# Kernel optimization log

Hardware: AMD Instinct MI355X
Metric: run time of the kernel (lower is better)

The kernel has to match this reference:

```python
import jax, jax.numpy as jnp
import numpy as np
import math

B, T, D, H, L = 64, 255, 512, 8, 8
CODEBOOK = 512
V = CODEBOOK + 3  # bos/eos/pad
COND_DIM = 512
MAX_LEN = 256
HD = D // H


def _layernorm(x, g, b, eps=1e-5):
    mu = jnp.mean(x, axis=-1, keepdims=True)
    var = jnp.mean(jnp.square(x - mu), axis=-1, keepdims=True)
    return (x - mu) * jax.lax.rsqrt(var + eps) * g + b


def setup_inputs() -> dict:
    key = jax.random.key(0)
    ks = jax.random.split(key, 24)
    s = 0.02
    d = {
        'tokens': jax.random.randint(ks[0], (B, T), 0, V),
        'cond': jax.random.normal(ks[1], (B, COND_DIM), jnp.float32),
        'emb': jax.random.normal(ks[2], (V, D), jnp.float32) * s,  # tied token_emb / head weight
        'pos_emb': jax.random.normal(ks[3], (1, MAX_LEN, D), jnp.float32) * s,
        'cond_w1': jax.random.normal(ks[4], (COND_DIM, D), jnp.float32) * s,
        'cond_b1': jnp.zeros((D,), jnp.float32),
        'cond_w2': jax.random.normal(ks[5], (D, D), jnp.float32) * s,
        'cond_b2': jnp.zeros((D,), jnp.float32),
        'ln1_g': jnp.ones((L, D), jnp.float32),
        'ln1_b': jnp.zeros((L, D), jnp.float32),
        'qkv_w': jax.random.normal(ks[6], (L, D, 3 * D), jnp.float32) * s,
        'qkv_b': jnp.zeros((L, 3 * D), jnp.float32),
        'proj_w': jax.random.normal(ks[7], (L, D, D), jnp.float32) * s,
        'proj_b': jnp.zeros((L, D), jnp.float32),
        'ln2_g': jnp.ones((L, D), jnp.float32),
        'ln2_b': jnp.zeros((L, D), jnp.float32),
        'mlp_w1': jax.random.normal(ks[8], (L, D, 4 * D), jnp.float32) * s,
        'mlp_b1': jnp.zeros((L, 4 * D), jnp.float32),
        'mlp_w2': jax.random.normal(ks[9], (L, 4 * D, D), jnp.float32) * s,
        'mlp_b2': jnp.zeros((L, D), jnp.float32),
        'lnf_g': jnp.ones((D,), jnp.float32),
        'lnf_b': jnp.zeros((D,), jnp.float32),
    }
    return d


def reference(tokens, cond, emb, pos_emb, cond_w1, cond_b1, cond_w2, cond_b2,
              ln1_g, ln1_b, qkv_w, qkv_b, proj_w, proj_b,
              ln2_g, ln2_b, mlp_w1, mlp_b1, mlp_w2, mlp_b2, lnf_g, lnf_b):
    b, t = tokens.shape
    h = emb[tokens] + pos_emb[:, :t, :]                              # [B,T,D]
    c = jax.nn.silu(cond @ cond_w1 + cond_b1) @ cond_w2 + cond_b2    # [B,D]
    h = jnp.concatenate([c[:, None, :], h], axis=1)                  # [B,S,D]
    S = t + 1
    causal = jnp.tril(jnp.ones((S, S), bool))
    scale = 1.0 / math.sqrt(HD)
    for i in range(L):
        x = _layernorm(h, ln1_g[i], ln1_b[i])
        qkv = (x @ qkv_w[i] + qkv_b[i]).reshape(b, S, 3, H, HD).transpose(2, 0, 3, 1, 4)
        q, k, v = qkv[0], qkv[1], qkv[2]                             # [B,H,S,hd]
        a = jnp.einsum('bhsd,bhtd->bhst', q, k) * scale
        a = jnp.where(causal, a, -jnp.inf)
        a = jax.nn.softmax(a, axis=-1)
        o = jnp.einsum('bhst,bhtd->bhsd', a, v).transpose(0, 2, 1, 3).reshape(b, S, D)
        h = h + o @ proj_w[i] + proj_b[i]
        x = _layernorm(h, ln2_g[i], ln2_b[i])
        h = h + jax.nn.gelu(x @ mlp_w1[i] + mlp_b1[i], approximate=False) @ mlp_w2[i] + mlp_b2[i]
    h = _layernorm(h, lnf_g, lnf_b)
    return (h @ emb.T)[:, 1:, :]                                     # [B,T,V]
```

## Files before the change

kernel.cpp:

```cpp
#include <hip/hip_runtime.h>
#include <hip/hip_bf16.h>

typedef __attribute__((ext_vector_type(8))) short bf16x8;
typedef __attribute__((ext_vector_type(4))) float f32x4;
typedef __attribute__((ext_vector_type(4))) unsigned short u16x4;
typedef __attribute__((ext_vector_type(8))) unsigned short u16x8;
typedef unsigned short u16;

#define DEV static __device__ __forceinline__

DEV float bf2f(u16 u) {
  union { unsigned int i; float f; } c; c.i = ((unsigned int)u) << 16; return c.f;
}
DEV u16 f2bf(float f) {
  union { float f; unsigned int i; } c; c.f = f;
  unsigned int i = c.i;
  i += 0x7FFFu + ((i >> 16) & 1u);
  return (u16)(i >> 16);
}

DEV void gload_lds16(const void* g, void* l) {
  __builtin_amdgcn_global_load_lds((const __attribute__((address_space(1))) void*)g,
                                   (__attribute__((address_space(3))) void*)l, 16, 0, 0);
}

DEV f32x4 mfma16(bf16x8 a, bf16x8 b, f32x4 c) {
  return __builtin_amdgcn_mfma_f32_16x16x32_bf16(a, b, c, 0, 0, 0);
}

DEV float fasterf(float x) {
  float ax = fabsf(x);
  float t = 1.0f / (1.0f + 0.3275911f * ax);
  float y = t * (0.254829592f + t * (-0.284496736f + t * (1.421413741f +
            t * (-1.453152027f + t * 1.061405429f))));
  float r = 1.0f - y * __expf(-ax * ax);
  return copysignf(r, x);
}
DEV float gelu(float v) { return 0.5f * v * (1.0f + fasterf(v * 0.70710678118f)); }

__global__ __launch_bounds__(256) void ktranspose(const float* __restrict__ in, u16* __restrict__ out,
                                                  int K, int N) {
  __shared__ u16 tile[32][33];
  const float* src = in + (size_t)blockIdx.z * K * N;
  u16* dst = out + (size_t)blockIdx.z * K * N;
  const int n0 = blockIdx.x * 32, k0 = blockIdx.y * 32;
  const int tx = threadIdx.x, ty = threadIdx.y;
#pragma unroll
  for (int i = ty; i < 32; i += 8) tile[i][tx] = f2bf(src[(size_t)(k0 + i) * N + n0 + tx]);
  __syncthreads();
#pragma unroll
  for (int i = ty; i < 32; i += 8) dst[(size_t)(n0 + i) * K + k0 + tx] = tile[tx][i];
}

__global__ __launch_bounds__(256) void kcvt(const float* __restrict__ in, u16* __restrict__ out, int n) {
  int i = blockIdx.x * 256 + threadIdx.x;
  if (i < n) out[i] = f2bf(in[i]);
}

__global__ __launch_bounds__(256) void kcond(const float* __restrict__ cond, const float* __restrict__ w1,
                                             const float* __restrict__ b1, const float* __restrict__ w2,
                                             const float* __restrict__ b2, float* __restrict__ h) {
  __shared__ float xr[512];
  __shared__ float t1[512];
  const int b = blockIdx.x, tid = threadIdx.x;
  for (int i = tid; i < 512; i += 256) xr[i] = cond[b * 512 + i];
  __syncthreads();
  for (int j = tid; j < 512; j += 256) {
    float acc = b1[j];
    for (int k = 0; k < 512; ++k) acc += xr[k] * w1[k * 512 + j];
    t1[j] = acc / (1.f + __expf(-acc));
  }
  __syncthreads();
  for (int j = tid; j < 512; j += 256) {
    float acc = b2[j];
    for (int k = 0; k < 512; ++k) acc += t1[k] * w2[k * 512 + j];
    h[(size_t)b * 256 * 512 + j] = acc;
  }
}

__global__ __launch_bounds__(256) void kembed(const int* __restrict__ tok, const float* __restrict__ emb,
                                              const float* __restrict__ pos, float* __restrict__ h) {
  const int idx = blockIdx.x;
  const int b = idx / 255, t = idx % 255;
  const int c = threadIdx.x * 2;
  const int tk = tok[idx];
  float2 ev = *(const float2*)(emb + (size_t)tk * 512 + c);
  float2 pv = *(const float2*)(pos + (size_t)t * 512 + c);
  float2 r;
  r.x = ev.x + pv.x;
  r.y = ev.y + pv.y;
  *(float2*)(h + ((size_t)b * 256 + 1 + t) * 512 + c) = r;
}

__global__ __launch_bounds__(256) void kln(const float* __restrict__ hin, const float* __restrict__ g,
                                           const float* __restrict__ bt, u16* __restrict__ out) {
  const int row = blockIdx.x * 4 + (threadIdx.x >> 6), lane = threadIdx.x & 63;
  const float4* x = (const float4*)(hin + (size_t)row * 512);
  float4 v0 = x[lane], v1 = x[lane + 64];
  float s1 = v0.x + v0.y + v0.z + v0.w + v1.x + v1.y + v1.z + v1.w;
  float s2 = v0.x * v0.x + v0.y * v0.y + v0.z * v0.z + v0.w * v0.w +
             v1.x * v1.x + v1.y * v1.y + v1.z * v1.z + v1.w * v1.w;
#pragma unroll
  for (int off = 1; off < 64; off <<= 1) { s1 += __shfl_xor(s1, off); s2 += __shfl_xor(s2, off); }
  float mu = s1 * (1.f / 512.f);
  float var = s2 * (1.f / 512.f) - mu * mu;
  float rs = rsqrtf(var + 1e-5f);
  const int c0 = lane * 4;
  float4 g0 = *(const float4*)(g + c0), g1 = *(const float4*)(g + 256 + c0);
  float4 b0 = *(const float4*)(bt + c0), b1 = *(const float4*)(bt + 256 + c0);
  u16x4 o0, o1;
  o0[0] = f2bf((v0.x - mu) * rs * g0.x + b0.x);
  o0[1] = f2bf((v0.y - mu) * rs * g0.y + b0.y);
  o0[2] = f2bf((v0.z - mu) * rs * g0.z + b0.z);
  o0[3] = f2bf((v0.w - mu) * rs * g0.w + b0.w);
  o1[0] = f2bf((v1.x - mu) * rs * g1.x + b1.x);
  o1[1] = f2bf((v1.y - mu) * rs * g1.y + b1.y);
  o1[2] = f2bf((v1.z - mu) * rs * g1.z + b1.z);
  o1[3] = f2bf((v1.w - mu) * rs * g1.w + b1.w);
  *(u16x4*)(out + (size_t)row * 512 + c0) = o0;
  *(u16x4*)(out + (size_t)row * 512 + 256 + c0) = o1;
}

template<int MODE>
__global__ __launch_bounds__(256, 2) void kgemm3(const u16* __restrict__ A, const u16* __restrict__ Bt,
                                                 const float* __restrict__ bias, void* __restrict__ Cout,
                                                 int M, int N, int K) {
  __shared__ __align__(16) u16 As[3][4096];
  __shared__ __align__(16) u16 Bs[3][4096];
  const int tid = threadIdx.x;
  const int lane = tid & 63;
  const int wr = tid >> 7, wc = (tid >> 6) & 1;
  const int m0 = blockIdx.x * 128, n0 = blockIdx.y * 128;
  const int nkt = K >> 5;
  const size_t Kb = (size_t)K * 2;

  const int srow = tid >> 2;
  const int schunk = tid & 3;
  const int sc = schunk ^ ((srow >> 1) & 3);
  const int d1 = tid * 16, d2 = tid * 16 + 4096;
  int brA = n0 + srow, brB = n0 + srow + 64;
  if (MODE == 3) { brA = min(brA, N - 1); brB = min(brB, N - 1); }
  const char* Ab = (const char*)A;
  const char* Bb = (const char*)Bt;
  const size_t a0 = (size_t)(m0 + srow) * Kb + sc * 16;
  const size_t a1 = (size_t)(m0 + srow + 64) * Kb + sc * 16;
  const size_t b0 = (size_t)brA * Kb + sc * 16;
  const size_t b1 = (size_t)brB * Kb + sc * 16;

  f32x4 acc[4][4];
#pragma unroll
  for (int i = 0; i < 4; ++i)
#pragma unroll
    for (int j = 0; j < 4; ++j) acc[i][j] = f32x4{0.f, 0.f, 0.f, 0.f};

#pragma unroll
  for (int t = 0; t < 2; ++t) {
    const size_t ko = (size_t)t * 64;
    gload_lds16(Ab + a0 + ko, (char*)As[t] + d1);
    gload_lds16(Ab + a1 + ko, (char*)As[t] + d2);
    gload_lds16(Bb + b0 + ko, (char*)Bs[t] + d1);
    gload_lds16(Bb + b1 + ko, (char*)Bs[t] + d2);
  }
  asm volatile("s_waitcnt vmcnt(4)" ::: "memory");
  __builtin_amdgcn_s_barrier();
  __builtin_amdgcn_sched_barrier(0);

  const int kchunk = (((lane >> 4) ^ ((lane >> 1) & 3)) << 4);
  const int arow = wr * 64 + (lane & 15);
  const int brow = wc * 64 + (lane & 15);

  for (int kt = 0; kt < nkt; ++kt) {
    const int bufc = kt % 3;
    const bool deep = (kt + 2 < nkt);
    if (deep) {
      const int bufn = (kt + 2) % 3;
      const size_t ko = (size_t)(kt + 2) * 64;
      gload_lds16(Ab + a0 + ko, (char*)As[bufn] + d1);
      gload_lds16(Ab + a1 + ko, (char*)As[bufn] + d2);
      gload_lds16(Bb + b0 + ko, (char*)Bs[bufn] + d1);
      gload_lds16(Bb + b1 + ko, (char*)Bs[bufn] + d2);
    }
    const char* Ap = (const char*)As[bufc];
    const char* Bp = (const char*)Bs[bufc];
    bf16x8 aF[4], bF[4];
#pragma unroll
    for (int mt = 0; mt < 4; ++mt) aF[mt] = *(const bf16x8*)(Ap + (arow + mt * 16) * 64 + kchunk);
#pragma unroll
    for (int nt = 0; nt < 4; ++nt) bF[nt] = *(const bf16x8*)(Bp + (brow + nt * 16) * 64 + kchunk);
#pragma unroll
    for (int mt = 0; mt < 4; ++mt)
#pragma unroll
      for (int nt = 0; nt < 4; ++nt)
        acc[mt][nt] = mfma16(aF[mt], bF[nt], acc[mt][nt]);
    if (deep) {
      asm volatile("s_waitcnt vmcnt(4)" ::: "memory");
    } else {
      asm volatile("s_waitcnt vmcnt(0)" ::: "memory");
    }
    __builtin_amdgcn_s_barrier();
    __builtin_amdgcn_sched_barrier(0);
  }

  float bv[4];
#pragma unroll
  for (int nt = 0; nt < 4; ++nt) {
    int col = n0 + wc * 64 + nt * 16 + (lane & 15);
    bv[nt] = (MODE == 3) ? 0.f : bias[col];
  }

  if (MODE == 0 || MODE == 1) {
    u16* C = (u16*)Cout;
#pragma unroll
    for (int mt = 0; mt < 4; ++mt)
#pragma unroll
      for (int r = 0; r < 4; ++r) {
        int row = m0 + wr * 64 + mt * 16 + (lane >> 4) * 4 + r;
        u16* cp = C + (size_t)row * N + n0 + wc * 64 + (lane & 15);
#pragma unroll
        for (int nt = 0; nt < 4; ++nt) {
          float v = acc[mt][nt][r] + bv[nt];
          if (MODE == 1) v = gelu(v);
          cp[nt * 16] = f2bf(v);
        }
      }
  } else if (MODE == 2) {
    float* hC = (float*)Cout;
#pragma unroll
    for (int mt = 0; mt < 4; ++mt)
#pragma unroll
      for (int r = 0; r < 4; ++r) {
        int row = m0 + wr * 64 + mt * 16 + (lane >> 4) * 4 + r;
        float* hp = hC + (size_t)row * N + n0 + wc * 64 + (lane & 15);
#pragma unroll
        for (int nt = 0; nt < 4; ++nt) hp[nt * 16] += acc[mt][nt][r] + bv[nt];
      }
  } else {
    float* C = (float*)Cout;
#pragma unroll
    for (int mt = 0; mt < 4; ++mt)
#pragma unroll
      for (int r = 0; r < 4; ++r) {
        int row = m0 + wr * 64 + mt * 16 + (lane >> 4) * 4 + r;
        int s = row & 255;
        if (s == 0) continue;
        int bb = row >> 8;
        float* cp = C + ((size_t)bb * 255 + (s - 1)) * 515 + n0 + wc * 64 + (lane & 15);
#pragma unroll
        for (int nt = 0; nt < 4; ++nt) {
          int col = n0 + wc * 64 + nt * 16 + (lane & 15);
          if (col < 515) cp[nt * 16] = acc[mt][nt][r];
        }
      }
  }
}

__global__ __launch_bounds__(256, 1) void kattn(const u16* __restrict__ qkv, u16* __restrict__ o) {
  __shared__ __align__(16) u16 Ks[256][72];
  __shared__ __align__(16) u16 Vt[64][264];
  __shared__ __align__(16) u16 Ps[4][64][72];
  const int tid = threadIdx.x, wv = tid >> 6, lane = tid & 63;
  const int bh = blockIdx.x, bb = bh >> 3, hh = bh & 7;
  const size_t base = (size_t)bb * 256 * 1536 + hh * 64;

  for (int c = tid; c < 2048; c += 256) {
    int s = c >> 3, pp = c & 7;
    u16x8 kv = *(const u16x8*)(qkv + base + (size_t)s * 1536 + 512 + pp * 8);
    *(u16x8*)&Ks[s][pp * 8] = kv;
    u16x8 vv = *(const u16x8*)(qkv + base + (size_t)s * 1536 + 1024 + pp * 8);
#pragma unroll
    for (int j = 0; j < 8; ++j) Vt[pp * 8 + j][s] = vv[j];
  }
  __syncthreads();

  bf16x8 qf[4][2];
#pragma unroll
  for (int mt = 0; mt < 4; ++mt)
#pragma unroll
    for (int ks = 0; ks < 2; ++ks)
      qf[mt][ks] = *(const bf16x8*)(qkv + base +
                   (size_t)(wv * 64 + mt * 16 + (lane & 15)) * 1536 + ks * 32 + (lane >> 4) * 8);

  const float scale = 0.125f;
  float mrow[4][4], lsum[4][4];
#pragma unroll
  for (int mt = 0; mt < 4; ++mt)
#pragma unroll
    for (int r = 0; r < 4; ++r) { mrow[mt][r] = -1e30f; lsum[mt][r] = 0.f; }

  for (int ct = 0; ct <= wv; ++ct) {
    f32x4 sacc[4][4];
#pragma unroll
    for (int i = 0; i < 4; ++i)
#pragma unroll
      for (int j = 0; j < 4; ++j) sacc[i][j] = f32x4{0.f, 0.f, 0.f, 0.f};
#pragma unroll
    for (int ks = 0; ks < 2; ++ks) {
      bf16x8 kf[4];
#pragma unroll
      for (int nt = 0; nt < 4; ++nt)
        kf[nt] = *(const bf16x8*)&Ks[ct * 64 + nt * 16 + (lane & 15)][ks * 32 + (lane >> 4) * 8];
#pragma unroll
      for (int mt = 0; mt < 4; ++mt)
#pragma unroll
        for (int nt = 0; nt < 4; ++nt)
          sacc[mt][nt] = mfma16(qf[mt][ks], kf[nt], sacc[mt][nt]);
    }
#pragma unroll
    for (int mt = 0; mt < 4; ++mt)
#pragma unroll
      for (int r = 0; r < 4; ++r) {
        int srow = wv * 64 + mt * 16 + (lane >> 4) * 4 + r;
        float mx = -1e30f;
#pragma unroll
        for (int nt = 0; nt < 4; ++nt) {
          int tcol = ct * 64 + nt * 16 + (lane & 15);
          float v = sacc[mt][nt][r] * scale;
          if (tcol > srow) v = -1e30f;
          mx = fmaxf(mx, v);
        }
#pragma unroll
        for (int off = 1; off < 16; off <<= 1) mx = fmaxf(mx, __shfl_xor(mx, off));
        mrow[mt][r] = fmaxf(mrow[mt][r], mx);
      }
  }

  f32x4 oacc[4][4];
#pragma unroll
  for (int i = 0; i < 4; ++i)
#pragma unroll
    for (int j = 0; j < 4; ++j) oacc[i][j] = f32x4{0.f, 0.f, 0.f, 0.f};

  for (int ct = 0; ct <= wv; ++ct) {
    f32x4 sacc[4][4];
#pragma unroll
    for (int i = 0; i < 4; ++i)
#pragma unroll
      for (int j = 0; j < 4; ++j) sacc[i][j] = f32x4{0.f, 0.f, 0.f, 0.f};
#pragma unroll
    for (int ks = 0; ks < 2; ++ks) {
      bf16x8 kf[4];
#pragma unroll
      for (int nt = 0; nt < 4; ++nt)
        kf[nt] = *(const bf16x8*)&Ks[ct * 64 + nt * 16 + (lane & 15)][ks * 32 + (lane >> 4) * 8];
#pragma unroll
      for (int mt = 0; mt < 4; ++mt)
#pragma unroll
        for (int nt = 0; nt < 4; ++nt)
          sacc[mt][nt] = mfma16(qf[mt][ks], kf[nt], sacc[mt][nt]);
    }
#pragma unroll
    for (int mt = 0; mt < 4; ++mt)
#pragma unroll
      for (int r = 0; r < 4; ++r) {
        int srow = wv * 64 + mt * 16 + (lane >> 4) * 4 + r;
        float ps = 0.f;
#pragma unroll
        for (int nt = 0; nt < 4; ++nt) {
          int tcol = ct * 64 + nt * 16 + (lane & 15);
          float v = sacc[mt][nt][r] * scale;
          float pe = (tcol > srow) ? 0.f : __expf(v - mrow[mt][r]);
          ps += pe;
          Ps[wv][mt * 16 + (lane >> 4) * 4 + r][nt * 16 + (lane & 15)] = f2bf(pe);
        }
#pragma unroll
        for (int off = 1; off < 16; off <<= 1) ps += __shfl_xor(ps, off);
        lsum[mt][r] += ps;
      }
#pragma unroll
    for (int ks = 0; ks < 2; ++ks) {
      bf16x8 pf[4], vf[4];
#pragma unroll
      for (int mt = 0; mt < 4; ++mt)
        pf[mt] = *(const bf16x8*)&Ps[wv][mt * 16 + (lane & 15)][ks * 32 + (lane >> 4) * 8];
#pragma unroll
      for (int nt = 0; nt < 4; ++nt)
        vf[nt] = *(const bf16x8*)&Vt[nt * 16 + (lane & 15)][ct * 64 + ks * 32 + (lane >> 4) * 8];
#pragma unroll
      for (int mt = 0; mt < 4; ++mt)
#pragma unroll
        for (int nt = 0; nt < 4; ++nt)
          oacc[mt][nt] = mfma16(pf[mt], vf[nt], oacc[mt][nt]);
    }
  }

#pragma unroll
  for (int mt = 0; mt < 4; ++mt)
#pragma unroll
    for (int r = 0; r < 4; ++r) {
      int s = wv * 64 + mt * 16 + (lane >> 4) * 4 + r;
      float inv = 1.f / lsum[mt][r];
      u16* op = o + ((size_t)bb * 256 + s) * 512 + hh * 64 + (lane & 15);
#pragma unroll
      for (int nt = 0; nt < 4; ++nt) op[nt * 16] = f2bf(oacc[mt][nt][r] * inv);
    }
}

extern "C" void kernel_launch(void* const* d_in, const int* in_sizes, int n_in,
                              void* d_out, int out_size, void* d_ws, size_t ws_size,
                              hipStream_t stream) {
  const int* tokens = (const int*)d_in[0];
  const float* cond = (const float*)d_in[1];
  const float* emb = (const float*)d_in[2];
  const float* pos = (const float*)d_in[3];
  const float* cw1 = (const float*)d_in[4];
  const float* cb1 = (const float*)d_in[5];
  const float* cw2 = (const float*)d_in[6];
  const float* cb2 = (const float*)d_in[7];
  const float* ln1g = (const float*)d_in[8];
  const float* ln1b = (const float*)d_in[9];
  const float* qkvw = (const float*)d_in[10];
  const float* qkvb = (const float*)d_in[11];
  const float* projw = (const float*)d_in[12];
  const float* projb = (const float*)d_in[13];
  const float* ln2g = (const float*)d_in[14];
  const float* ln2b = (const float*)d_in[15];
  const float* w1 = (const float*)d_in[16];
  const float* b1 = (const float*)d_in[17];
  const float* w2 = (const float*)d_in[18];
  const float* b2 = (const float*)d_in[19];
  const float* lnfg = (const float*)d_in[20];
  const float* lnfb = (const float*)d_in[21];

  const size_t NEEDED = (size_t)16384 * 512 * 4
                      + (size_t)16384 * 512 * 2
                      + (size_t)16384 * 2048 * 2
                      + (size_t)8 * 1536 * 512 * 2
                      + (size_t)8 * 512 * 512 * 2
                      + (size_t)8 * 2048 * 512 * 2
                      + (size_t)8 * 512 * 2048 * 2;
  if (ws_size < NEEDED) return;

  char* p = (char*)d_ws;
  float* h = (float*)p;        p += (size_t)16384 * 512 * 4;
  u16* xln = (u16*)p;          p += (size_t)16384 * 512 * 2;
  u16* big = (u16*)p;          p += (size_t)16384 * 2048 * 2;
  u16* attn_o = big + (size_t)16384 * 1536;
  u16* embB = big;
  u16* qkvT = (u16*)p;         p += (size_t)8 * 1536 * 512 * 2;
  u16* projT = (u16*)p;        p += (size_t)8 * 512 * 512 * 2;
  u16* w1T = (u16*)p;          p += (size_t)8 * 2048 * 512 * 2;
  u16* w2T = (u16*)p;          p += (size_t)8 * 512 * 2048 * 2;

  ktranspose<<<dim3(48, 16, 8), dim3(32, 8), 0, stream>>>(qkvw, qkvT, 512, 1536);
  ktranspose<<<dim3(16, 16, 8), dim3(32, 8), 0, stream>>>(projw, projT, 512, 512);
  ktranspose<<<dim3(64, 16, 8), dim3(32, 8), 0, stream>>>(w1, w1T, 512, 2048);
  ktranspose<<<dim3(16, 64, 8), dim3(32, 8), 0, stream>>>(w2, w2T, 2048, 512);

  kembed<<<16320, 256, 0, stream>>>(tokens, emb, pos, h);
  kcond<<<64, 256, 0, stream>>>(cond, cw1, cb1, cw2, cb2, h);

  for (int l = 0; l < 8; ++l) {
    kln<<<4096, 256, 0, stream>>>(h, ln1g + l * 512, ln1b + l * 512, xln);
    kgemm3<0><<<dim3(128, 12), 256, 0, stream>>>(xln, qkvT + (size_t)l * 1536 * 512,
                                                 qkvb + l * 1536, big, 16384, 1536, 512);
    kattn<<<512, 256, 0, stream>>>(big, attn_o);
    kgemm3<2><<<dim3(128, 4), 256, 0, stream>>>(attn_o, projT + (size_t)l * 512 * 512,
                                                projb + l * 512, h, 16384, 512, 512);
    kln<<<4096, 256, 0, stream>>>(h, ln2g + l * 512, ln2b + l * 512, xln);
    kgemm3<1><<<dim3(128, 16), 256, 0, stream>>>(xln, w1T + (size_t)l * 2048 * 512,
                                                 b1 + l * 2048, big, 16384, 2048, 512);
    kgemm3<2><<<dim3(128, 4), 256, 0, stream>>>(big, w2T + (size_t)l * 512 * 2048,
                                                b2 + l * 512, h, 16384, 512, 2048);
  }
  kln<<<4096, 256, 0, stream>>>(h, lnfg, lnfb, xln);
  kcvt<<<1030, 256, 0, stream>>>(emb, embB, 515 * 512);
  kgemm3<3><<<dim3(128, 5), 256, 0, stream>>>(xln, embB, nullptr, d_out, 16384, 515, 512);
}
```

Before: 2.104 ms.

## Add 8-wave GEMM with larger tiles and interleaved load/MFMA schedule for layer GEMMs

Adds a new 512-thread GEMM kernel with 256-wide N tiles and 256- or 128-row M tiles, double-buffered LDS with XOR swizzle, and a ping-pong schedule. The schedule interleaves global-to-LDS loads of the next B tile and the tile after for A between MFMA half-steps, using barriers and s_setprio to favour MFMA issue. All four per-layer GEMMs switch to it, while the old kernel stays only for the final vocab projection. The goal is more data reuse per block and better overlap of memory traffic with matrix math. The cost is heavier LDS use and more barriers per K step, which may limit occupancy.

Result: faster. 1.973 ms (-6.2%).

```diff
diff --git a/kernel.cpp b/kernel.cpp
--- a/kernel.cpp
+++ b/kernel.cpp
@@ -27,6 +27,8 @@
 DEV f32x4 mfma16(bf16x8 a, bf16x8 b, f32x4 c) {
   return __builtin_amdgcn_mfma_f32_16x16x32_bf16(a, b, c, 0, 0, 0);
 }
+
+template<int N> DEV void vwait() { asm volatile("s_waitcnt vmcnt(%0)" :: "n"(N) : "memory"); }
 
 DEV float fasterf(float x) {
   float ax = fabsf(x);
@@ -121,6 +123,169 @@
   *(u16x4*)(out + (size_t)row * 512 + 256 + c0) = o1;
 }
 
+template<int MODE, int FM>
+__global__ __launch_bounds__(512, 2) void kgemm8(const u16* __restrict__ A, const u16* __restrict__ Bt,
+                                                 const float* __restrict__ bias, void* __restrict__ Cout,
+                                                 int M, int N, int K) {
+  constexpr int BM = FM * 32;
+  constexpr int ABYTES = BM * 128;
+  constexpr int BBYTES = 256 * 128;
+  constexpr int AH = ABYTES / 2, BH = BBYTES / 2;
+  constexpr int ALD = AH / 8192;
+  constexpr int BOFF = 2 * ABYTES;
+  __shared__ __align__(16) char shm[2 * ABYTES + 2 * BBYTES];
+
+  const int tid = threadIdx.x;
+  const int lane = tid & 63;
+  const int wid = tid >> 6;
+  const int wr = wid >> 2;
+  const int wc = wid & 3;
+  const int fr = lane & 15, fq = lane >> 4;
+  const int axor = (fr & 7) << 4;
+  const int m0 = blockIdx.x * BM, n0 = blockIdx.y * 256;
+  const int nkt = K >> 6;
+  const int Kb = K * 2;
+  const char* Ab = (const char*)A;
+  const char* Bb = (const char*)Bt;
+
+  unsigned aOff[2][ALD], bOff[2][2];
+#pragma unroll
+  for (int h = 0; h < 2; ++h) {
+#pragma unroll
+    for (int j = 0; j < ALD; ++j) {
+      int d = h * AH + j * 8192 + tid * 16;
+      int row = d >> 7, pc = (d >> 4) & 7;
+      aOff[h][j] = (unsigned)((m0 + row) * Kb + ((pc ^ (row & 7)) << 4));
+    }
+#pragma unroll
+    for (int j = 0; j < 2; ++j) {
+      int d = h * BH + j * 8192 + tid * 16;
+      int row = d >> 7, pc = (d >> 4) & 7;
+      bOff[h][j] = (unsigned)((n0 + row) * Kb + ((pc ^ (row & 7)) << 4));
+    }
+  }
+
+  auto stA = [&](int kt, int h, int b) {
+#pragma unroll
+    for (int j = 0; j < ALD; ++j)
+      gload_lds16(Ab + (size_t)aOff[h][j] + (size_t)kt * 128,
+                  shm + b * ABYTES + h * AH + j * 8192 + tid * 16);
+  };
+  auto stB = [&](int kt, int h, int b) {
+#pragma unroll
+    for (int j = 0; j < 2; ++j)
+      gload_lds16(Bb + (size_t)bOff[h][j] + (size_t)kt * 128,
+                  shm + BOFF + b * BBYTES + h * BH + j * 8192 + tid * 16);
+  };
+  auto rdA = [&](int b, int m, int ks) {
+    return *(const bf16x8*)(shm + b * ABYTES + (wr * (BM / 2) + m * 16 + fr) * 128 +
+                            ((ks * 64 + fq * 16) ^ axor));
+  };
+  auto rdB = [&](int b, int n, int ks) {
+    return *(const bf16x8*)(shm + BOFF + b * BBYTES + (wc * 64 + n * 16 + fr) * 128 +
+                            ((ks * 64 + fq * 16) ^ axor));
+  };
+
+  f32x4 acc[FM][4];
+#pragma unroll
+  for (int i = 0; i < FM; ++i)
+#pragma unroll
+    for (int j = 0; j < 4; ++j) acc[i][j] = f32x4{0.f, 0.f, 0.f, 0.f};
+
+  stA(0, 0, 0); stA(0, 1, 0); stB(0, 0, 0); stB(0, 1, 0);
+  if (nkt > 1) { stA(1, 0, 1); stA(1, 1, 1); }
+  vwait<2 * ALD>();
+  __builtin_amdgcn_sched_barrier(0);
+  __builtin_amdgcn_s_barrier();
+
+  for (int kt = 0; kt < nkt; ++kt) {
+    const int cur = kt & 1;
+    const bool sb = (kt + 1 < nkt);
+    const bool sa = (kt + 2 < nkt);
+    bf16x8 aF[FM][2], bF[4][2];
+#pragma unroll
+    for (int m = 0; m < FM; ++m) aF[m][0] = rdA(cur, m, 0);
+#pragma unroll
+    for (int n = 0; n < 4; ++n) bF[n][0] = rdB(cur, n, 0);
+    if (sb) stB(kt + 1, 0, cur ^ 1);
+    __builtin_amdgcn_s_barrier();
+    __builtin_amdgcn_s_setprio(1);
+#pragma unroll
+    for (int m = 0; m < FM / 2; ++m)
+#pragma unroll
+      for (int n = 0; n < 4; ++n) acc[m][n] = mfma16(aF[m][0], bF[n][0], acc[m][n]);
+    __builtin_amdgcn_s_setprio(0);
+    __builtin_amdgcn_s_barrier();
+#pragma unroll
+    for (int m = 0; m < FM; ++m) aF[m][1] = rdA(cur, m, 1);
+#pragma unroll
+    for (int n = 0; n < 4; ++n) bF[n][1] = rdB(cur, n, 1);
+    if (sb) stB(kt + 1, 1, cur ^ 1);
+    __builtin_amdgcn_s_barrier();
+    __builtin_amdgcn_s_setprio(1);
+#pragma unroll
+    for (int m = FM / 2; m < FM; ++m)
+#pragma unroll
+      for (int n = 0; n < 4; ++n) acc[m][n] = mfma16(aF[m][0], bF[n][0], acc[m][n]);
+    __builtin_amdgcn_s_setprio(0);
+    asm volatile("s_waitcnt lgkmcnt(0)" ::: "memory");
+    __builtin_amdgcn_sched_barrier(0);
+    __builtin_amdgcn_s_barrier();
+    if (sa) stA(kt + 2, 0, cur);
+    __builtin_amdgcn_s_barrier();
+    __builtin_amdgcn_s_setprio(1);
+#pragma unroll
+    for (int m = 0; m < FM / 2; ++m)
+#pragma unroll
+      for (int n = 0; n < 4; ++n) acc[m][n] = mfma16(aF[m][1], bF[n][1], acc[m][n]);
+    __builtin_amdgcn_s_setprio(0);
+    __builtin_amdgcn_s_barrier();
+    if (sa) stA(kt + 2, 1, cur);
+    __builtin_amdgcn_s_barrier();
+    __builtin_amdgcn_s_setprio(1);
+#pragma unroll
+    for (int m = FM / 2; m < FM; ++m)
+#pragma unroll
+      for (int n = 0; n < 4; ++n) acc[m][n] = mfma16(aF[m][1], bF[n][1], acc[m][n]);
+    __builtin_amdgcn_s_setprio(0);
+    if (sa) vwait<2 * ALD>(); else vwait<0>();
+    __builtin_amdgcn_sched_barrier(0);
+    __builtin_amdgcn_s_barrier();
+  }
+
+  float bv[4];
+#pragma unroll
+  for (int n = 0; n < 4; ++n) bv[n] = bias[n0 + wc * 64 + n * 16 + fr];
+
+  if (MODE == 0 || MODE == 1) {
+    u16* C = (u16*)Cout;
+#pragma unroll
+    for (int m = 0; m < FM; ++m)
+#pragma unroll
+      for (int r = 0; r < 4; ++r) {
+        int row = m0 + wr * (BM / 2) + m * 16 + fq * 4 + r;
+        u16* cp = C + (size_t)row * N + n0 + wc * 64 + fr;
+#pragma unroll
+        for (int n = 0; n < 4; ++n) {
+          float v = acc[m][n][r] + bv[n];
+          if (MODE == 1) v = gelu(v);
+          cp[n * 16] = f2bf(v);
+        }
+      }
+  } else {
+    float* hC = (float*)Cout;
+#pragma unroll
+    for (int m = 0; m < FM; ++m)
+#pragma unroll
+      for (int r = 0; r < 4; ++r) {
+        int row = m0 + wr * (BM / 2) + m * 16 + fq * 4 + r;
+        float* hp = hC + (size_t)row * N + n0 + wc * 64 + fr;
+#pragma unroll
+        for (int n = 0; n < 4; ++n) hp[n * 16] += acc[m][n][r] + bv[n];
+      }
+  }
+}
+
 template<int MODE>
 __global__ __launch_bounds__(256, 2) void kgemm3(const u16* __restrict__ A, const u16* __restrict__ Bt,
                                                  const float* __restrict__ bias, void* __restrict__ Cout,
@@ -201,40 +366,7 @@
     __builtin_amdgcn_sched_barrier(0);
   }
 
-  float bv[4];
-#pragma unroll
-  for (int nt = 0; nt < 4; ++nt) {
-    int col = n0 + wc * 64 + nt * 16 + (lane & 15);
-    bv[nt] = (MODE == 3) ? 0.f : bias[col];
-  }
-
-  if (MODE == 0 || MODE == 1) {
-    u16* C = (u16*)Cout;
-#pragma unroll
-    for (int mt = 0; mt < 4; ++mt)
-#pragma unroll
-      for (int r = 0; r < 4; ++r) {
-        int row = m0 + wr * 64 + mt * 16 + (lane >> 4) * 4 + r;
-        u16* cp = C + (size_t)row * N + n0 + wc * 64 + (lane & 15);
-#pragma unroll
-        for (int nt = 0; nt < 4; ++nt) {
-          float v = acc[mt][nt][r] + bv[nt];
-          if (MODE == 1) v = gelu(v);
-          cp[nt * 16] = f2bf(v);
-        }
-      }
-  } else if (MODE == 2) {
-    float* hC = (float*)Cout;
-#pragma unroll
-    for (int mt = 0; mt < 4; ++mt)
-#pragma unroll
-      for (int r = 0; r < 4; ++r) {
-        int row = m0 + wr * 64 + mt * 16 + (lane >> 4) * 4 + r;
-        float* hp = hC + (size_t)row * N + n0 + wc * 64 + (lane & 15);
-#pragma unroll
-        for (int nt = 0; nt < 4; ++nt) hp[nt * 16] += acc[mt][nt][r] + bv[nt];
-      }
-  } else {
+  if (MODE == 3) {
     float* C = (float*)Cout;
 #pragma unroll
     for (int mt = 0; mt < 4; ++mt)
@@ -451,16 +583,16 @@
 
   for (int l = 0; l < 8; ++l) {
     kln<<<4096, 256, 0, stream>>>(h, ln1g + l * 512, ln1b + l * 512, xln);
-    kgemm3<0><<<dim3(128, 12), 256, 0, stream>>>(xln, qkvT + (size_t)l * 1536 * 512,
-                                                 qkvb + l * 1536, big, 16384, 1536, 512);
+    kgemm8<0, 8><<<dim3(64, 6), 512, 0, stream>>>(xln, qkvT + (size_t)l * 1536 * 512,
+                                                  qkvb + l * 1536, big, 16384, 1536, 512);
     kattn<<<512, 256, 0, stream>>>(big, attn_o);
-    kgemm3<2><<<dim3(128, 4), 256, 0, stream>>>(attn_o, projT + (size_t)l * 512 * 512,
-                                                projb + l * 512, h, 16384, 512, 512);
+    kgemm8<2, 4><<<dim3(128, 2), 512, 0, stream>>>(attn_o, projT + (size_t)l * 512 * 512,
+                                                   projb + l * 512, h, 16384, 512, 512);
     kln<<<4096, 256, 0, stream>>>(h, ln2g + l * 512, ln2b + l * 512, xln);
-    kgemm3<1><<<dim3(128, 16), 256, 0, stream>>>(xln, w1T + (size_t)l * 2048 * 512,
-                                                 b1 + l * 2048, big, 16384, 2048, 512);
-    kgemm3<2><<<dim3(128, 4), 256, 0, stream>>>(big, w2T + (size_t)l * 512 * 2048,
-                                                b2 + l * 512, h, 16384, 512, 2048);
+    kgemm8<1, 8><<<dim3(64, 8), 512, 0, stream>>>(xln, w1T + (size_t)l * 2048 * 512,
+                                                  b1 + l * 2048, big, 16384, 2048, 512);
+    kgemm8<2, 4><<<dim3(128, 2), 512, 0, stream>>>(big, w2T + (size_t)l * 512 * 2048,
+                                                   b2 + l * 512, h, 16384, 512, 2048);
   }
   kln<<<4096, 256, 0, stream>>>(h, lnfg, lnfb, xln);
   kcvt<<<1030, 256, 0, stream>>>(emb, embB, 515 * 512);
```
